# Optimization experiments

Hardware: AMD Instinct MI355X
Metric: run time of the kernel (lower is better)

The kernel has to match this reference:

```python
import jax, jax.numpy as jnp
import numpy as np

# Model/config constants
N = 2048          # total nodes in batch
G = 32            # number of graphs
NPG = 64          # nodes per graph (N = G * NPG)
E = 16384         # total edges (E//G per graph, unique within graph)
HIDDEN = 256
N_HEADS = 8
HEAD_DIM = HIDDEN // N_HEADS
EDGE_FEAT = 16
SCALE = HEAD_DIM ** -0.5


def setup_inputs() -> dict:
    key = jax.random.key(0)
    ks = jax.random.split(key, 16)
    nodes = jax.random.normal(ks[0], (N, HIDDEN), dtype=jnp.float32)
    edges = jax.random.normal(ks[1], (E, EDGE_FEAT), dtype=jnp.float32)
    n_node = jnp.full((G,), NPG, dtype=jnp.int32)
    # Unique (sender, receiver) pairs within each graph block
    epg = E // G
    gkeys = jax.random.split(ks[2], G)
    perm = jax.vmap(lambda k: jax.random.permutation(k, NPG * NPG)[:epg])(gkeys)  # [G, epg]
    so = perm // NPG
    ro = perm % NPG
    base = (jnp.arange(G, dtype=jnp.int32) * NPG)[:, None]
    senders = (base + so).reshape(-1).astype(jnp.int32)
    receivers = (base + ro).reshape(-1).astype(jnp.int32)
    init = 0.02
    Wq = jax.random.normal(ks[3], (HIDDEN, HIDDEN), jnp.float32) * init
    Wk = jax.random.normal(ks[4], (HIDDEN, HIDDEN), jnp.float32) * init
    Wv = jax.random.normal(ks[5], (HIDDEN, HIDDEN), jnp.float32) * init
    Wo = jax.random.normal(ks[6], (HIDDEN, HIDDEN), jnp.float32) * init
    We = jax.random.normal(ks[7], (EDGE_FEAT, N_HEADS), jnp.float32) * init
    bq = jnp.zeros((HIDDEN,), jnp.float32)
    bk = jnp.zeros((HIDDEN,), jnp.float32)
    bv = jnp.zeros((HIDDEN,), jnp.float32)
    bo = jnp.zeros((HIDDEN,), jnp.float32)
    be = jnp.zeros((N_HEADS,), jnp.float32)
    return {"nodes": nodes, "edges": edges, "n_node": n_node,
            "senders": senders, "receivers": receivers,
            "Wq": Wq, "bq": bq, "Wk": Wk, "bk": bk, "Wv": Wv, "bv": bv,
            "Wo": Wo, "bo": bo, "We": We, "be": be}


def reference(nodes, edges, n_node, senders, receivers,
              Wq, bq, Wk, bk, Wv, bv, Wo, bo, We, be):
    n_nodes = nodes.shape[0]
    n_graphs = n_node.shape[0]
    q = (nodes @ Wq + bq).reshape(n_nodes, N_HEADS, HEAD_DIM)
    k = (nodes @ Wk + bk).reshape(n_nodes, N_HEADS, HEAD_DIM)
    v = (nodes @ Wv + bv).reshape(n_nodes, N_HEADS, HEAD_DIM)
    scores = jnp.einsum('ihd,jhd->ijh', q, k) * SCALE  # [N, N, H]
    graph_idx = jnp.repeat(jnp.arange(n_graphs), n_node, total_repeat_length=n_nodes)
    same_graph = graph_idx[:, None] == graph_idx[None, :]
    scores = scores + jnp.where(same_graph[:, :, None], 0.0, -1e9)
    # Edge bias scattered into [N, N, H] at (receiver, sender)
    edge_bias = edges @ We + be  # [E, H]
    edge_bias_matrix = jnp.zeros((n_nodes, n_nodes, N_HEADS), dtype=scores.dtype)
    edge_bias_matrix = edge_bias_matrix.at[receivers, senders].set(edge_bias)
    scores = scores + edge_bias_matrix
    attn = jax.nn.softmax(scores, axis=1)  # softmax over key axis j
    out = jnp.einsum('ijh,jhd->ihd', attn, v).reshape(n_nodes, HIDDEN)
    return out @ Wo + bo
```

## Files before the change

### kernel.cpp

```cpp
#include <hip/hip_runtime.h>

#define N_NODES 2048
#define N_GRAPHS 32
#define NPG 64
#define N_EDGES 16384
#define EPG 512
#define HIDDEN 256
#define NHEADS 8
#define HEADDIM 32
#define EDGEFEAT 16
#define ATT_SCALE 0.17677669529663687f

typedef unsigned short u16;
typedef __attribute__((ext_vector_type(8))) short bf16x8;
typedef __attribute__((ext_vector_type(4))) float f32x4;

__device__ __forceinline__ u16 f2b(float f) {
    unsigned x = __float_as_uint(f);
    return (u16)((x + 0x7fffu + ((x >> 16) & 1u)) >> 16);
}
__device__ __forceinline__ float b2f(u16 u) {
    return __uint_as_float(((unsigned)u) << 16);
}
__device__ __forceinline__ unsigned pack2(float a, float b) {
    return (unsigned)f2b(a) | ((unsigned)f2b(b) << 16);
}

__global__ __launch_bounds__(256)
void qkv_attn_fused(const float* __restrict__ nodes,
                    const float* __restrict__ Wq, const float* __restrict__ Wk,
                    const float* __restrict__ Wv,
                    const float* __restrict__ bq, const float* __restrict__ bk,
                    const float* __restrict__ bv,
                    const float* __restrict__ edges, const float* __restrict__ We,
                    const float* __restrict__ be,
                    const int* __restrict__ senders, const int* __restrict__ receivers,
                    u16* __restrict__ attnb)
{
    const int g = blockIdx.x, h = blockIdx.y;
    const int tid = threadIdx.x;
    const int lane = tid & 63, wv = tid >> 6;
    const int l16 = lane & 15, quad = lane >> 4;

    __shared__ __align__(16) unsigned char smem[84480];
    short* An = (short*)smem;
    short* Wt = (short*)smem + 64 * 264;
    short* qhi = (short*)smem;
    short* qlo = qhi + 64 * 40;
    short* khi = qlo + 64 * 40;
    short* klo = khi + 64 * 40;
    short* vsT = klo + 64 * 40;
    float* sc  = (float*)(smem + 25088);
    float* red = sc + 64 * 65;
    __shared__ float we_h[EDGEFEAT];
    __shared__ float sbe;

    if (tid < EDGEFEAT) we_h[tid] = We[tid * NHEADS + h];
    if (tid == 0) sbe = be[h];

    #pragma unroll
    for (int rep = 0; rep < 16; ++rep) {
        const int q = rep * 256 + tid;
        const int row = q >> 6, f4 = q & 63;
        float4 x = *(const float4*)(nodes + (size_t)(g * NPG + row) * HIDDEN + f4 * 4);
        *(uint2*)&An[row * 264 + f4 * 4] = make_uint2(pack2(x.x, x.y), pack2(x.z, x.w));
    }
    #pragma unroll
    for (int rep = 0; rep < 24; ++rep) {
        const int q = rep * 256 + tid;
        const float* Wp = (rep < 8) ? Wq : (rep < 16) ? Wk : Wv;
        const int r = q & 2047;
        const int krow = r >> 3, f4 = r & 7;
        float4 x = *(const float4*)(Wp + (size_t)krow * HIDDEN + h * HEADDIM + f4 * 4);
        const int nb = (rep >> 3) * 32 + f4 * 4;
        Wt[(nb + 0) * 264 + krow] = (short)f2b(x.x);
        Wt[(nb + 1) * 264 + krow] = (short)f2b(x.y);
        Wt[(nb + 2) * 264 + krow] = (short)f2b(x.z);
        Wt[(nb + 3) * 264 + krow] = (short)f2b(x.w);
    }
    __syncthreads();

    f32x4 acc[6];
    #pragma unroll
    for (int nt = 0; nt < 6; ++nt) acc[nt] = (f32x4){0.f, 0.f, 0.f, 0.f};
    const int arow = (wv * 16 + l16) * 264 + quad * 8;
    #pragma unroll
    for (int k0 = 0; k0 < HIDDEN; k0 += 32) {
        bf16x8 af = *(const bf16x8*)&An[arow + k0];
        #pragma unroll
        for (int nt = 0; nt < 6; ++nt) {
            bf16x8 bf = *(const bf16x8*)&Wt[(nt * 16 + l16) * 264 + k0 + quad * 8];
            acc[nt] = __builtin_amdgcn_mfma_f32_16x16x32_bf16(af, bf, acc[nt], 0, 0, 0);
        }
    }
    __syncthreads();

    #pragma unroll
    for (int nt = 0; nt < 6; ++nt) {
        const int tns = nt >> 1;
        const int col = (nt & 1) * 16 + l16;
        const float* bp = (tns == 0) ? bq : (tns == 1) ? bk : bv;
        const float bias = bp[h * HEADDIM + col];
        #pragma unroll
        for (int r = 0; r < 4; ++r) {
            const int row = wv * 16 + quad * 4 + r;
            const float val = acc[nt][r] + bias;
            if (tns == 2) {
                vsT[col * 72 + row] = (short)f2b(val);
            } else {
                const u16 hi = f2b(val);
                const u16 lo = f2b(val - b2f(hi));
                if (tns == 0) { qhi[row * 40 + col] = (short)hi; qlo[row * 40 + col] = (short)lo; }
                else          { khi[row * 40 + col] = (short)hi; klo[row * 40 + col] = (short)lo; }
            }
        }
    }
    __syncthreads();

    {
        bf16x8 qh = *(const bf16x8*)&qhi[(wv * 16 + l16) * 40 + quad * 8];
        bf16x8 ql = *(const bf16x8*)&qlo[(wv * 16 + l16) * 40 + quad * 8];
        #pragma unroll
        for (int nt = 0; nt < 4; ++nt) {
            bf16x8 kh = *(const bf16x8*)&khi[(nt * 16 + l16) * 40 + quad * 8];
            bf16x8 kl = *(const bf16x8*)&klo[(nt * 16 + l16) * 40 + quad * 8];
            f32x4 s = (f32x4){0.f, 0.f, 0.f, 0.f};
            s = __builtin_amdgcn_mfma_f32_16x16x32_bf16(qh, kh, s, 0, 0, 0);
            s = __builtin_amdgcn_mfma_f32_16x16x32_bf16(qh, kl, s, 0, 0, 0);
            s = __builtin_amdgcn_mfma_f32_16x16x32_bf16(ql, kh, s, 0, 0, 0);
            #pragma unroll
            for (int r = 0; r < 4; ++r)
                sc[(wv * 16 + quad * 4 + r) * 65 + nt * 16 + l16] = s[r] * ATT_SCALE;
        }
    }
    __syncthreads();

    #pragma unroll
    for (int rep = 0; rep < 2; ++rep) {
        const int e = g * EPG + rep * 256 + tid;
        const float* ef = edges + (size_t)e * EDGEFEAT;
        float4 f0 = *(const float4*)(ef + 0);
        float4 f1 = *(const float4*)(ef + 4);
        float4 f2 = *(const float4*)(ef + 8);
        float4 f3 = *(const float4*)(ef + 12);
        float b = sbe
            + f0.x * we_h[0]  + f0.y * we_h[1]  + f0.z * we_h[2]  + f0.w * we_h[3]
            + f1.x * we_h[4]  + f1.y * we_h[5]  + f1.z * we_h[6]  + f1.w * we_h[7]
            + f2.x * we_h[8]  + f2.y * we_h[9]  + f2.z * we_h[10] + f2.w * we_h[11]
            + f3.x * we_h[12] + f3.y * we_h[13] + f3.z * we_h[14] + f3.w * we_h[15];
        const int s_l = senders[e] & (NPG - 1);
        const int r_l = receivers[e] & (NPG - 1);
        sc[r_l * 65 + s_l] += b;
    }
    __syncthreads();

    {
        const int i  = tid & 63;
        const int cg = tid >> 6;
        float* red_m = red;
        float* red_s = red + 4 * 64;
        float m = -1e30f;
        #pragma unroll
        for (int jj = 0; jj < 16; ++jj) m = fmaxf(m, sc[i * 65 + cg * 16 + jj]);
        red_m[cg * 64 + i] = m;
        __syncthreads();
        m = fmaxf(fmaxf(red_m[0 * 64 + i], red_m[1 * 64 + i]),
                  fmaxf(red_m[2 * 64 + i], red_m[3 * 64 + i]));
        float s = 0.f;
        #pragma unroll
        for (int jj = 0; jj < 16; ++jj) {
            const int j = cg * 16 + jj;
            float e = __expf(sc[i * 65 + j] - m);
            sc[i * 65 + j] = e;
            s += e;
        }
        red_s[cg * 64 + i] = s;
        __syncthreads();
        const float inv = 1.f / (red_s[0 * 64 + i] + red_s[1 * 64 + i] +
                                 red_s[2 * 64 + i] + red_s[3 * 64 + i]);
        #pragma unroll
        for (int jj = 0; jj < 16; ++jj) sc[i * 65 + cg * 16 + jj] *= inv;
    }
    __syncthreads();

    {
        f32x4 oacc[2];
        oacc[0] = (f32x4){0.f, 0.f, 0.f, 0.f};
        oacc[1] = (f32x4){0.f, 0.f, 0.f, 0.f};
        #pragma unroll
        for (int k0 = 0; k0 < NPG; k0 += 32) {
            float p[8];
            #pragma unroll
            for (int jj = 0; jj < 8; ++jj)
                p[jj] = sc[(wv * 16 + l16) * 65 + k0 + quad * 8 + jj];
            uint4 uh, ul;
            u16 h0 = f2b(p[0]), h1 = f2b(p[1]), h2 = f2b(p[2]), h3 = f2b(p[3]);
            u16 h4 = f2b(p[4]), h5 = f2b(p[5]), h6 = f2b(p[6]), h7 = f2b(p[7]);
            uh.x = (unsigned)h0 | ((unsigned)h1 << 16);
            uh.y = (unsigned)h2 | ((unsigned)h3 << 16);
            uh.z = (unsigned)h4 | ((unsigned)h5 << 16);
            uh.w = (unsigned)h6 | ((unsigned)h7 << 16);
            ul.x = pack2(p[0] - b2f(h0), p[1] - b2f(h1));
            ul.y = pack2(p[2] - b2f(h2), p[3] - b2f(h3));
            ul.z = pack2(p[4] - b2f(h4), p[5] - b2f(h5));
            ul.w = pack2(p[6] - b2f(h6), p[7] - b2f(h7));
            bf16x8 ph = *(bf16x8*)&uh;
            bf16x8 pl = *(bf16x8*)&ul;
            #pragma unroll
            for (int nt = 0; nt < 2; ++nt) {
                bf16x8 vf = *(const bf16x8*)&vsT[(nt * 16 + l16) * 72 + k0 + quad * 8];
                oacc[nt] = __builtin_amdgcn_mfma_f32_16x16x32_bf16(ph, vf, oacc[nt], 0, 0, 0);
                oacc[nt] = __builtin_amdgcn_mfma_f32_16x16x32_bf16(pl, vf, oacc[nt], 0, 0, 0);
            }
        }
        #pragma unroll
        for (int nt = 0; nt < 2; ++nt) {
            const int d = nt * 16 + l16;
            #pragma unroll
            for (int r = 0; r < 4; ++r) {
                const int row = wv * 16 + quad * 4 + r;
                attnb[(size_t)(g * NPG + row) * HIDDEN + h * HEADDIM + d] =
                    f2b(oacc[nt][r]);
            }
        }
    }
}

__global__ __launch_bounds__(256)
void outproj_fused(const u16* __restrict__ A,
                   const float* __restrict__ Wo,
                   const float* __restrict__ bo,
                   float* __restrict__ C)
{
    const int n0 = blockIdx.x * 64, m0 = blockIdx.y * 64;
    const int tid = threadIdx.x;
    const int lane = tid & 63, wv = tid >> 6;
    const int l16 = lane & 15, quad = lane >> 4;

    __shared__ __align__(16) short Ab[64 * 264];
    __shared__ __align__(16) short Bb[64 * 264];

    #pragma unroll
    for (int rep = 0; rep < 8; ++rep) {
        const int q = rep * 256 + tid;
        const int row = q >> 5, u = q & 31;
        *(uint4*)&Ab[row * 264 + u * 8] =
            *(const uint4*)(A + (size_t)(m0 + row) * HIDDEN + u * 8);
    }
    #pragma unroll
    for (int rep = 0; rep < 16; ++rep) {
        const int q = rep * 256 + tid;
        const int f4 = q & 7;
        const int krow = (q >> 3) & 255;
        const int half = q >> 11;
        float4 x = *(const float4*)(Wo + (size_t)krow * HIDDEN + n0 + half * 32 + f4 * 4);
        const int nb = half * 32 + f4 * 4;
        Bb[(nb + 0) * 264 + krow] = (short)f2b(x.x);
        Bb[(nb + 1) * 264 + krow] = (short)f2b(x.y);
        Bb[(nb + 2) * 264 + krow] = (short)f2b(x.z);
        Bb[(nb + 3) * 264 + krow] = (short)f2b(x.w);
    }
    __syncthreads();

    f32x4 acc[4];
    #pragma unroll
    for (int nt = 0; nt < 4; ++nt) acc[nt] = (f32x4){0.f, 0.f, 0.f, 0.f};
    const int arow = (wv * 16 + l16) * 264 + quad * 8;
    #pragma unroll
    for (int k0 = 0; k0 < HIDDEN; k0 += 32) {
        bf16x8 af = *(const bf16x8*)&Ab[arow + k0];
        #pragma unroll
        for (int nt = 0; nt < 4; ++nt) {
            bf16x8 bf = *(const bf16x8*)&Bb[(nt * 16 + l16) * 264 + k0 + quad * 8];
            acc[nt] = __builtin_amdgcn_mfma_f32_16x16x32_bf16(af, bf, acc[nt], 0, 0, 0);
        }
    }

    #pragma unroll
    for (int nt = 0; nt < 4; ++nt) {
        const int col = n0 + nt * 16 + l16;
        const float bias = bo[col];
        #pragma unroll
        for (int r = 0; r < 4; ++r)
            C[(size_t)(m0 + wv * 16 + quad * 4 + r) * HIDDEN + col] = acc[nt][r] + bias;
    }
}

extern "C" void kernel_launch(void* const* d_in, const int* in_sizes, int n_in,
                              void* d_out, int out_size, void* d_ws, size_t ws_size,
                              hipStream_t stream)
{
    const float* nodes     = (const float*)d_in[0];
    const float* edges     = (const float*)d_in[1];
    const int*   senders   = (const int*)d_in[3];
    const int*   receivers = (const int*)d_in[4];
    const float* Wq = (const float*)d_in[5];
    const float* bq = (const float*)d_in[6];
    const float* Wk = (const float*)d_in[7];
    const float* bk = (const float*)d_in[8];
    const float* Wv = (const float*)d_in[9];
    const float* bv = (const float*)d_in[10];
    const float* Wo = (const float*)d_in[11];
    const float* bo = (const float*)d_in[12];
    const float* We = (const float*)d_in[13];
    const float* be = (const float*)d_in[14];
    float* out = (float*)d_out;

    u16* attnb = (u16*)d_ws;

    qkv_attn_fused<<<dim3(N_GRAPHS, NHEADS), dim3(256), 0, stream>>>(
        nodes, Wq, Wk, Wv, bq, bk, bv, edges, We, be, senders, receivers, attnb);
    outproj_fused<<<dim3(HIDDEN / 64, N_NODES / 64), dim3(256), 0, stream>>>(
        attnb, Wo, bo, out);
}
```

Baseline: 93.70 us.

## Fuse attention and output projection into one cooperative kernel with grid sync

Merges the per-graph/head attention kernel and the output projection GEMM into a single cooperative launch of 256 blocks, separated by a grid-wide barrier. The second phase re-tiles the out-projection to 64x32 tiles so it uses the same 256 blocks. This removes one kernel launch and the inter-kernel gap, at the cost of a grid sync and smaller GEMM tiles that reload the A tile more often.

```diff
diff --git a/kernel.cpp b/kernel.cpp
--- a/kernel.cpp
+++ b/kernel.cpp
@@ -1,4 +1,7 @@
 #include <hip/hip_runtime.h>
+#include <hip/hip_cooperative_groups.h>
+
+namespace cg = cooperative_groups;
 
 #define N_NODES 2048
 #define N_GRAPHS 32
@@ -27,262 +30,263 @@
 }
 
 __global__ __launch_bounds__(256)
-void qkv_attn_fused(const float* __restrict__ nodes,
-                    const float* __restrict__ Wq, const float* __restrict__ Wk,
-                    const float* __restrict__ Wv,
-                    const float* __restrict__ bq, const float* __restrict__ bk,
-                    const float* __restrict__ bv,
-                    const float* __restrict__ edges, const float* __restrict__ We,
-                    const float* __restrict__ be,
-                    const int* __restrict__ senders, const int* __restrict__ receivers,
-                    u16* __restrict__ attnb)
+void fused_all(const float* __restrict__ nodes,
+               const float* __restrict__ Wq, const float* __restrict__ Wk,
+               const float* __restrict__ Wv,
+               const float* __restrict__ bq, const float* __restrict__ bk,
+               const float* __restrict__ bv,
+               const float* __restrict__ edges, const float* __restrict__ We,
+               const float* __restrict__ be,
+               const int* __restrict__ senders, const int* __restrict__ receivers,
+               const float* __restrict__ Wo, const float* __restrict__ bo,
+               u16* __restrict__ attnb,
+               float* __restrict__ out)
 {
-    const int g = blockIdx.x, h = blockIdx.y;
+    const int bid = blockIdx.x;
     const int tid = threadIdx.x;
     const int lane = tid & 63, wv = tid >> 6;
     const int l16 = lane & 15, quad = lane >> 4;
 
     __shared__ __align__(16) unsigned char smem[84480];
-    short* An = (short*)smem;
-    short* Wt = (short*)smem + 64 * 264;
-    short* qhi = (short*)smem;
-    short* qlo = qhi + 64 * 40;
-    short* khi = qlo + 64 * 40;
-    short* klo = khi + 64 * 40;
-    short* vsT = klo + 64 * 40;
-    float* sc  = (float*)(smem + 25088);
-    float* red = sc + 64 * 65;
     __shared__ float we_h[EDGEFEAT];
     __shared__ float sbe;
 
-    if (tid < EDGEFEAT) we_h[tid] = We[tid * NHEADS + h];
-    if (tid == 0) sbe = be[h];
-
-    #pragma unroll
-    for (int rep = 0; rep < 16; ++rep) {
-        const int q = rep * 256 + tid;
-        const int row = q >> 6, f4 = q & 63;
-        float4 x = *(const float4*)(nodes + (size_t)(g * NPG + row) * HIDDEN + f4 * 4);
-        *(uint2*)&An[row * 264 + f4 * 4] = make_uint2(pack2(x.x, x.y), pack2(x.z, x.w));
-    }
-    #pragma unroll
-    for (int rep = 0; rep < 24; ++rep) {
-        const int q = rep * 256 + tid;
-        const float* Wp = (rep < 8) ? Wq : (rep < 16) ? Wk : Wv;
-        const int r = q & 2047;
-        const int krow = r >> 3, f4 = r & 7;
-        float4 x = *(const float4*)(Wp + (size_t)krow * HIDDEN + h * HEADDIM + f4 * 4);
-        const int nb = (rep >> 3) * 32 + f4 * 4;
-        Wt[(nb + 0) * 264 + krow] = (short)f2b(x.x);
-        Wt[(nb + 1) * 264 + krow] = (short)f2b(x.y);
-        Wt[(nb + 2) * 264 + krow] = (short)f2b(x.z);
-        Wt[(nb + 3) * 264 + krow] = (short)f2b(x.w);
-    }
-    __syncthreads();
-
-    f32x4 acc[6];
-    #pragma unroll
-    for (int nt = 0; nt < 6; ++nt) acc[nt] = (f32x4){0.f, 0.f, 0.f, 0.f};
-    const int arow = (wv * 16 + l16) * 264 + quad * 8;
-    #pragma unroll
-    for (int k0 = 0; k0 < HIDDEN; k0 += 32) {
-        bf16x8 af = *(const bf16x8*)&An[arow + k0];
+    {
+        const int g = bid & 31, h = bid >> 5;
+
+        short* An = (short*)smem;
+        short* Wt = (short*)smem + 64 * 264;
+        short* qhi = (short*)smem;
+        short* qlo = qhi + 64 * 40;
+        short* khi = qlo + 64 * 40;
+        short* klo = khi + 64 * 40;
+        short* vsT = klo + 64 * 40;
+        float* sc  = (float*)(smem + 25088);
+        float* red = sc + 64 * 65;
+
+        if (tid < EDGEFEAT) we_h[tid] = We[tid * NHEADS + h];
+        if (tid == 0) sbe = be[h];
+
+        #pragma unroll
+        for (int rep = 0; rep < 16; ++rep) {
+            const int q = rep * 256 + tid;
+            const int row = q >> 6, f4 = q & 63;
+            float4 x = *(const float4*)(nodes + (size_t)(g * NPG + row) * HIDDEN + f4 * 4);
+            *(uint2*)&An[row * 264 + f4 * 4] = make_uint2(pack2(x.x, x.y), pack2(x.z, x.w));
+        }
+        #pragma unroll
+        for (int rep = 0; rep < 24; ++rep) {
+            const int q = rep * 256 + tid;
+            const float* Wp = (rep < 8) ? Wq : (rep < 16) ? Wk : Wv;
+            const int r = q & 2047;
+            const int krow = r >> 3, f4 = r & 7;
+            float4 x = *(const float4*)(Wp + (size_t)krow * HIDDEN + h * HEADDIM + f4 * 4);
+            const int nb = (rep >> 3) * 32 + f4 * 4;
+            Wt[(nb + 0) * 264 + krow] = (short)f2b(x.x);
+            Wt[(nb + 1) * 264 + krow] = (short)f2b(x.y);
+            Wt[(nb + 2) * 264 + krow] = (short)f2b(x.z);
+            Wt[(nb + 3) * 264 + krow] = (short)f2b(x.w);
+        }
+        __syncthreads();
+
+        f32x4 acc[6];
+        #pragma unroll
+        for (int nt = 0; nt < 6; ++nt) acc[nt] = (f32x4){0.f, 0.f, 0.f, 0.f};
+        const int arow = (wv * 16 + l16) * 264 + quad * 8;
+        #pragma unroll
+        for (int k0 = 0; k0 < HIDDEN; k0 += 32) {
+            bf16x8 af = *(const bf16x8*)&An[arow + k0];
+            #pragma unroll
+            for (int nt = 0; nt < 6; ++nt) {
+                bf16x8 bf = *(const bf16x8*)&Wt[(nt * 16 + l16) * 264 + k0 + quad * 8];
+                acc[nt] = __builtin_amdgcn_mfma_f32_16x16x32_bf16(af, bf, acc[nt], 0, 0, 0);
+            }
+        }
+        __syncthreads();
+
         #pragma unroll
         for (int nt = 0; nt < 6; ++nt) {
-            bf16x8 bf = *(const bf16x8*)&Wt[(nt * 16 + l16) * 264 + k0 + quad * 8];
-            acc[nt] = __builtin_amdgcn_mfma_f32_16x16x32_bf16(af, bf, acc[nt], 0, 0, 0);
-        }
-    }
-    __syncthreads();
-
-    #pragma unroll
-    for (int nt = 0; nt < 6; ++nt) {
-        const int tns = nt >> 1;
-        const int col = (nt & 1) * 16 + l16;
-        const float* bp = (tns == 0) ? bq : (tns == 1) ? bk : bv;
-        const float bias = bp[h * HEADDIM + col];
-        #pragma unroll
-        for (int r = 0; r < 4; ++r) {
-            const int row = wv * 16 + quad * 4 + r;
-            const float val = acc[nt][r] + bias;
-            if (tns == 2) {
-                vsT[col * 72 + row] = (short)f2b(val);
-            } else {
-                const u16 hi = f2b(val);
-                const u16 lo = f2b(val - b2f(hi));
-                if (tns == 0) { qhi[row * 40 + col] = (short)hi; qlo[row * 40 + col] = (short)lo; }
-                else          { khi[row * 40 + col] = (short)hi; klo[row * 40 + col] = (short)lo; }
-            }
-        }
-    }
-    __syncthreads();
-
-    {
-        bf16x8 qh = *(const bf16x8*)&qhi[(wv * 16 + l16) * 40 + quad * 8];
-        bf16x8 ql = *(const bf16x8*)&qlo[(wv * 16 + l16) * 40 + quad * 8];
-        #pragma unroll
-        for (int nt = 0; nt < 4; ++nt) {
-            bf16x8 kh = *(const bf16x8*)&khi[(nt * 16 + l16) * 40 + quad * 8];
-            bf16x8 kl = *(const bf16x8*)&klo[(nt * 16 + l16) * 40 + quad * 8];
-            f32x4 s = (f32x4){0.f, 0.f, 0.f, 0.f};
-            s = __builtin_amdgcn_mfma_f32_16x16x32_bf16(qh, kh, s, 0, 0, 0);
-            s = __builtin_amdgcn_mfma_f32_16x16x32_bf16(qh, kl, s, 0, 0, 0);
-            s = __builtin_amdgcn_mfma_f32_16x16x32_bf16(ql, kh, s, 0, 0, 0);
-            #pragma unroll
-            for (int r = 0; r < 4; ++r)
-                sc[(wv * 16 + quad * 4 + r) * 65 + nt * 16 + l16] = s[r] * ATT_SCALE;
-        }
-    }
-    __syncthreads();
-
-    #pragma unroll
-    for (int rep = 0; rep < 2; ++rep) {
-        const int e = g * EPG + rep * 256 + tid;
-        const float* ef = edges + (size_t)e * EDGEFEAT;
-        float4 f0 = *(const float4*)(ef + 0);
-        float4 f1 = *(const float4*)(ef + 4);
-        float4 f2 = *(const float4*)(ef + 8);
-        float4 f3 = *(const float4*)(ef + 12);
-        float b = sbe
-            + f0.x * we_h[0]  + f0.y * we_h[1]  + f0.z * we_h[2]  + f0.w * we_h[3]
-            + f1.x * we_h[4]  + f1.y * we_h[5]  + f1.z * we_h[6]  + f1.w * we_h[7]
-            + f2.x * we_h[8]  + f2.y * we_h[9]  + f2.z * we_h[10] + f2.w * we_h[11]
-            + f3.x * we_h[12] + f3.y * we_h[13] + f3.z * we_h[14] + f3.w * we_h[15];
-        const int s_l = senders[e] & (NPG - 1);
-        const int r_l = receivers[e] & (NPG - 1);
-        sc[r_l * 65 + s_l] += b;
-    }
-    __syncthreads();
-
-    {
-        const int i  = tid & 63;
-        const int cg = tid >> 6;
-        float* red_m = red;
-        float* red_s = red + 4 * 64;
-        float m = -1e30f;
-        #pragma unroll
-        for (int jj = 0; jj < 16; ++jj) m = fmaxf(m, sc[i * 65 + cg * 16 + jj]);
-        red_m[cg * 64 + i] = m;
-        __syncthreads();
-        m = fmaxf(fmaxf(red_m[0 * 64 + i], red_m[1 * 64 + i]),
-                  fmaxf(red_m[2 * 64 + i], red_m[3 * 64 + i]));
-        float s = 0.f;
-        #pragma unroll
-        for (int jj = 0; jj < 16; ++jj) {
-            const int j = cg * 16 + jj;
-            float e = __expf(sc[i * 65 + j] - m);
-            sc[i * 65 + j] = e;
-            s += e;
-        }
-        red_s[cg * 64 + i] = s;
-        __syncthreads();
-        const float inv = 1.f / (red_s[0 * 64 + i] + red_s[1 * 64 + i] +
-                                 red_s[2 * 64 + i] + red_s[3 * 64 + i]);
-        #pragma unroll
-        for (int jj = 0; jj < 16; ++jj) sc[i * 65 + cg * 16 + jj] *= inv;
-    }
-    __syncthreads();
-
-    {
-        f32x4 oacc[2];
-        oacc[0] = (f32x4){0.f, 0.f, 0.f, 0.f};
-        oacc[1] = (f32x4){0.f, 0.f, 0.f, 0.f};
-        #pragma unroll
-        for (int k0 = 0; k0 < NPG; k0 += 32) {
-            float p[8];
-            #pragma unroll
-            for (int jj = 0; jj < 8; ++jj)
-                p[jj] = sc[(wv * 16 + l16) * 65 + k0 + quad * 8 + jj];
-            uint4 uh, ul;
-            u16 h0 = f2b(p[0]), h1 = f2b(p[1]), h2 = f2b(p[2]), h3 = f2b(p[3]);
-            u16 h4 = f2b(p[4]), h5 = f2b(p[5]), h6 = f2b(p[6]), h7 = f2b(p[7]);
-            uh.x = (unsigned)h0 | ((unsigned)h1 << 16);
-            uh.y = (unsigned)h2 | ((unsigned)h3 << 16);
-            uh.z = (unsigned)h4 | ((unsigned)h5 << 16);
-            uh.w = (unsigned)h6 | ((unsigned)h7 << 16);
-            ul.x = pack2(p[0] - b2f(h0), p[1] - b2f(h1));
-            ul.y = pack2(p[2] - b2f(h2), p[3] - b2f(h3));
-            ul.z = pack2(p[4] - b2f(h4), p[5] - b2f(h5));
-            ul.w = pack2(p[6] - b2f(h6), p[7] - b2f(h7));
-            bf16x8 ph = *(bf16x8*)&uh;
-            bf16x8 pl = *(bf16x8*)&ul;
-            #pragma unroll
-            for (int nt = 0; nt < 2; ++nt) {
-                bf16x8 vf = *(const bf16x8*)&vsT[(nt * 16 + l16) * 72 + k0 + quad * 8];
-                oacc[nt] = __builtin_amdgcn_mfma_f32_16x16x32_bf16(ph, vf, oacc[nt], 0, 0, 0);
-                oacc[nt] = __builtin_amdgcn_mfma_f32_16x16x32_bf16(pl, vf, oacc[nt], 0, 0, 0);
-            }
-        }
-        #pragma unroll
-        for (int nt = 0; nt < 2; ++nt) {
-            const int d = nt * 16 + l16;
+            const int tns = nt >> 1;
+            const int col = (nt & 1) * 16 + l16;
+            const float* bp = (tns == 0) ? bq : (tns == 1) ? bk : bv;
+            const float bias = bp[h * HEADDIM + col];
             #pragma unroll
             for (int r = 0; r < 4; ++r) {
                 const int row = wv * 16 + quad * 4 + r;
-                attnb[(size_t)(g * NPG + row) * HIDDEN + h * HEADDIM + d] =
-                    f2b(oacc[nt][r]);
+                const float val = acc[nt][r] + bias;
+                if (tns == 2) {
+                    vsT[col * 72 + row] = (short)f2b(val);
+                } else {
+                    const u16 hi = f2b(val);
+                    const u16 lo = f2b(val - b2f(hi));
+                    if (tns == 0) { qhi[row * 40 + col] = (short)hi; qlo[row * 40 + col] = (short)lo; }
+                    else          { khi[row * 40 + col] = (short)hi; klo[row * 40 + col] = (short)lo; }
+                }
+            }
+        }
+        __syncthreads();
+
+        {
+            bf16x8 qh = *(const bf16x8*)&qhi[(wv * 16 + l16) * 40 + quad * 8];
+            bf16x8 ql = *(const bf16x8*)&qlo[(wv * 16 + l16) * 40 + quad * 8];
+            #pragma unroll
+            for (int nt = 0; nt < 4; ++nt) {
+                bf16x8 kh = *(const bf16x8*)&khi[(nt * 16 + l16) * 40 + quad * 8];
+                bf16x8 kl = *(const bf16x8*)&klo[(nt * 16 + l16) * 40 + quad * 8];
+                f32x4 s = (f32x4){0.f, 0.f, 0.f, 0.f};
+                s = __builtin_amdgcn_mfma_f32_16x16x32_bf16(qh, kh, s, 0, 0, 0);
+                s = __builtin_amdgcn_mfma_f32_16x16x32_bf16(qh, kl, s, 0, 0, 0);
+                s = __builtin_amdgcn_mfma_f32_16x16x32_bf16(ql, kh, s, 0, 0, 0);
+                #pragma unroll
+                for (int r = 0; r < 4; ++r)
+                    sc[(wv * 16 + quad * 4 + r) * 65 + nt * 16 + l16] = s[r] * ATT_SCALE;
+            }
+        }
+        __syncthreads();
+
+        #pragma unroll
+        for (int rep = 0; rep < 2; ++rep) {
+            const int e = g * EPG + rep * 256 + tid;
+            const float* ef = edges + (size_t)e * EDGEFEAT;
+            float4 f0 = *(const float4*)(ef + 0);
+            float4 f1 = *(const float4*)(ef + 4);
+            float4 f2 = *(const float4*)(ef + 8);
+            float4 f3 = *(const float4*)(ef + 12);
+            float b = sbe
+                + f0.x * we_h[0]  + f0.y * we_h[1]  + f0.z * we_h[2]  + f0.w * we_h[3]
+                + f1.x * we_h[4]  + f1.y * we_h[5]  + f1.z * we_h[6]  + f1.w * we_h[7]
+                + f2.x * we_h[8]  + f2.y * we_h[9]  + f2.z * we_h[10] + f2.w * we_h[11]
+                + f3.x * we_h[12] + f3.y * we_h[13] + f3.z * we_h[14] + f3.w * we_h[15];
+            const int s_l = senders[e] & (NPG - 1);
+            const int r_l = receivers[e] & (NPG - 1);
+            sc[r_l * 65 + s_l] += b;
+        }
+        __syncthreads();
+
+        {
+            const int i  = tid & 63;
+            const int cg_ = tid >> 6;
+            float* red_m = red;
+            float* red_s = red + 4 * 64;
+            float m = -1e30f;
+            #pragma unroll
+            for (int jj = 0; jj < 16; ++jj) m = fmaxf(m, sc[i * 65 + cg_ * 16 + jj]);
+            red_m[cg_ * 64 + i] = m;
+            __syncthreads();
+            m = fmaxf(fmaxf(red_m[0 * 64 + i], red_m[1 * 64 + i]),
+                      fmaxf(red_m[2 * 64 + i], red_m[3 * 64 + i]));
+            float s = 0.f;
+            #pragma unroll
+            for (int jj = 0; jj < 16; ++jj) {
+                const int j = cg_ * 16 + jj;
+                float e = __expf(sc[i * 65 + j] - m);
+                sc[i * 65 + j] = e;
+                s += e;
+            }
+            red_s[cg_ * 64 + i] = s;
+            __syncthreads();
+            const float inv = 1.f / (red_s[0 * 64 + i] + red_s[1 * 64 + i] +
+                                     red_s[2 * 64 + i] + red_s[3 * 64 + i]);
+            #pragma unroll
+            for (int jj = 0; jj < 16; ++jj) sc[i * 65 + cg_ * 16 + jj] *= inv;
+        }
+        __syncthreads();
+
+        {
+            f32x4 oacc[2];
+            oacc[0] = (f32x4){0.f, 0.f, 0.f, 0.f};
+            oacc[1] = (f32x4){0.f, 0.f, 0.f, 0.f};
+            #pragma unroll
+            for (int k0 = 0; k0 < NPG; k0 += 32) {
+                float p[8];
+                #pragma unroll
+                for (int jj = 0; jj < 8; ++jj)
+                    p[jj] = sc[(wv * 16 + l16) * 65 + k0 + quad * 8 + jj];
+                uint4 uh, ul;
+                u16 h0 = f2b(p[0]), h1 = f2b(p[1]), h2 = f2b(p[2]), h3 = f2b(p[3]);
+                u16 h4 = f2b(p[4]), h5 = f2b(p[5]), h6 = f2b(p[6]), h7 = f2b(p[7]);
+                uh.x = (unsigned)h0 | ((unsigned)h1 << 16);
+                uh.y = (unsigned)h2 | ((unsigned)h3 << 16);
+                uh.z = (unsigned)h4 | ((unsigned)h5 << 16);
+                uh.w = (unsigned)h6 | ((unsigned)h7 << 16);
+                ul.x = pack2(p[0] - b2f(h0), p[1] - b2f(h1));
+                ul.y = pack2(p[2] - b2f(h2), p[3] - b2f(h3));
+                ul.z = pack2(p[4] - b2f(h4), p[5] - b2f(h5));
+                ul.w = pack2(p[6] - b2f(h6), p[7] - b2f(h7));
+                bf16x8 ph = *(bf16x8*)&uh;
+                bf16x8 pl = *(bf16x8*)&ul;
+                #pragma unroll
+                for (int nt = 0; nt < 2; ++nt) {
+                    bf16x8 vf = *(const bf16x8*)&vsT[(nt * 16 + l16) * 72 + k0 + quad * 8];
+                    oacc[nt] = __builtin_amdgcn_mfma_f32_16x16x32_bf16(ph, vf, oacc[nt], 0, 0, 0);
+                    oacc[nt] = __builtin_amdgcn_mfma_f32_16x16x32_bf16(pl, vf, oacc[nt], 0, 0, 0);
+                }
+            }
+            #pragma unroll
+            for (int nt = 0; nt < 2; ++nt) {
+                const int d = nt * 16 + l16;
+                #pragma unroll
+                for (int r = 0; r < 4; ++r) {
+                    const int row = wv * 16 + quad * 4 + r;
+                    attnb[(size_t)(g * NPG + row) * HIDDEN + h * HEADDIM + d] =
+                        f2b(oacc[nt][r]);
+                }
             }
         }
     }
-}
-
-__global__ __launch_bounds__(256)
-void outproj_fused(const u16* __restrict__ A,
-                   const float* __restrict__ Wo,
-                   const float* __restrict__ bo,
-                   float* __restrict__ C)
-{
-    const int n0 = blockIdx.x * 64, m0 = blockIdx.y * 64;
-    const int tid = threadIdx.x;
-    const int lane = tid & 63, wv = tid >> 6;
-    const int l16 = lane & 15, quad = lane >> 4;
-
-    __shared__ __align__(16) short Ab[64 * 264];
-    __shared__ __align__(16) short Bb[64 * 264];
-
-    #pragma unroll
-    for (int rep = 0; rep < 8; ++rep) {
-        const int q = rep * 256 + tid;
-        const int row = q >> 5, u = q & 31;
-        *(uint4*)&Ab[row * 264 + u * 8] =
-            *(const uint4*)(A + (size_t)(m0 + row) * HIDDEN + u * 8);
-    }
-    #pragma unroll
-    for (int rep = 0; rep < 16; ++rep) {
-        const int q = rep * 256 + tid;
-        const int f4 = q & 7;
-        const int krow = (q >> 3) & 255;
-        const int half = q >> 11;
-        float4 x = *(const float4*)(Wo + (size_t)krow * HIDDEN + n0 + half * 32 + f4 * 4);
-        const int nb = half * 32 + f4 * 4;
-        Bb[(nb + 0) * 264 + krow] = (short)f2b(x.x);
-        Bb[(nb + 1) * 264 + krow] = (short)f2b(x.y);
-        Bb[(nb + 2) * 264 + krow] = (short)f2b(x.z);
-        Bb[(nb + 3) * 264 + krow] = (short)f2b(x.w);
-    }
-    __syncthreads();
-
-    f32x4 acc[4];
-    #pragma unroll
-    for (int nt = 0; nt < 4; ++nt) acc[nt] = (f32x4){0.f, 0.f, 0.f, 0.f};
-    const int arow = (wv * 16 + l16) * 264 + quad * 8;
-    #pragma unroll
-    for (int k0 = 0; k0 < HIDDEN; k0 += 32) {
-        bf16x8 af = *(const bf16x8*)&Ab[arow + k0];
-        #pragma unroll
-        for (int nt = 0; nt < 4; ++nt) {
-            bf16x8 bf = *(const bf16x8*)&Bb[(nt * 16 + l16) * 264 + k0 + quad * 8];
-            acc[nt] = __builtin_amdgcn_mfma_f32_16x16x32_bf16(af, bf, acc[nt], 0, 0, 0);
-        }
-    }
-
-    #pragma unroll
-    for (int nt = 0; nt < 4; ++nt) {
-        const int col = n0 + nt * 16 + l16;
-        const float bias = bo[col];
-        #pragma unroll
-        for (int r = 0; r < 4; ++r)
-            C[(size_t)(m0 + wv * 16 + quad * 4 + r) * HIDDEN + col] = acc[nt][r] + bias;
+
+    cg::this_grid().sync();
+
+    {
+        const int m0 = (bid & 31) * 64;
+        const int n0 = (bid >> 5) * 32;
+
+        short* Ab = (short*)smem;
+        short* Bb = (short*)smem + 64 * 264;
+
+        #pragma unroll
+        for (int rep = 0; rep < 8; ++rep) {
+            const int q = rep * 256 + tid;
+            const int row = q >> 5, u = q & 31;
+            *(uint4*)&Ab[row * 264 + u * 8] =
+                *(const uint4*)(attnb + (size_t)(m0 + row) * HIDDEN + u * 8);
+        }
+        #pragma unroll
+        for (int rep = 0; rep < 8; ++rep) {
+            const int q = rep * 256 + tid;
+            const int krow = q >> 3, f4 = q & 7;
+            float4 x = *(const float4*)(Wo + (size_t)krow * HIDDEN + n0 + f4 * 4);
+            const int nb = f4 * 4;
+            Bb[(nb + 0) * 264 + krow] = (short)f2b(x.x);
+            Bb[(nb + 1) * 264 + krow] = (short)f2b(x.y);
+            Bb[(nb + 2) * 264 + krow] = (short)f2b(x.z);
+            Bb[(nb + 3) * 264 + krow] = (short)f2b(x.w);
+        }
+        __syncthreads();
+
+        f32x4 acc[2];
+        acc[0] = (f32x4){0.f, 0.f, 0.f, 0.f};
+        acc[1] = (f32x4){0.f, 0.f, 0.f, 0.f};
+        const int arow = (wv * 16 + l16) * 264 + quad * 8;
+        #pragma unroll
+        for (int k0 = 0; k0 < HIDDEN; k0 += 32) {
+            bf16x8 af = *(const bf16x8*)&Ab[arow + k0];
+            #pragma unroll
+            for (int nt = 0; nt < 2; ++nt) {
+                bf16x8 bf = *(const bf16x8*)&Bb[(nt * 16 + l16) * 264 + k0 + quad * 8];
+                acc[nt] = __builtin_amdgcn_mfma_f32_16x16x32_bf16(af, bf, acc[nt], 0, 0, 0);
+            }
+        }
+
+        #pragma unroll
+        for (int nt = 0; nt < 2; ++nt) {
+            const int col = n0 + nt * 16 + l16;
+            const float bias = bo[col];
+            #pragma unroll
+            for (int r = 0; r < 4; ++r)
+                out[(size_t)(m0 + wv * 16 + quad * 4 + r) * HIDDEN + col] =
+                    acc[nt][r] + bias;
+        }
     }
 }
 
@@ -308,8 +312,13 @@
 
     u16* attnb = (u16*)d_ws;
 
-    qkv_attn_fused<<<dim3(N_GRAPHS, NHEADS), dim3(256), 0, stream>>>(
-        nodes, Wq, Wk, Wv, bq, bk, bv, edges, We, be, senders, receivers, attnb);
-    outproj_fused<<<dim3(HIDDEN / 64, N_NODES / 64), dim3(256), 0, stream>>>(
-        attnb, Wo, bo, out);
-}
+    void* args[] = {
+        (void*)&nodes, (void*)&Wq, (void*)&Wk, (void*)&Wv,
+        (void*)&bq, (void*)&bk, (void*)&bv,
+        (void*)&edges, (void*)&We, (void*)&be,
+        (void*)&senders, (void*)&receivers,
+        (void*)&Wo, (void*)&bo, (void*)&attnb, (void*)&out
+    };
+    hipLaunchCooperativeKernel((const void*)fused_all, dim3(256), dim3(256),
+                               args, 0, stream);
+}
```

After: 151.2 us. +61.3%, slower.

## Load node fragments directly into registers and prefetch edge data early

Applied to the files above, without the earlier changes.

The QKV projection now builds the bf16 A fragments straight from global memory into registers, so the node tile is no longer staged through shared memory. That staging cut lets the LDS allocation shrink. Edge features and sender/receiver indices are loaded at kernel start so their latency overlaps the weight staging and the matmuls. Shared-memory strides for the transposed weight and V tiles change to odd-word padding (266/74) to reduce bank conflicts on the transposed stores. The risk is that 16-byte vector LDS reads at those strides are no longer 16-byte aligned, and more registers stay live.

```diff
diff --git a/kernel.cpp b/kernel.cpp
--- a/kernel.cpp
+++ b/kernel.cpp
@@ -10,6 +10,10 @@
 #define HEADDIM 32
 #define EDGEFEAT 16
 #define ATT_SCALE 0.17677669529663687f
+
+#define WT_S 266
+#define VS_S 74
+#define QK_S 40
 
 typedef unsigned short u16;
 typedef __attribute__((ext_vector_type(8))) short bf16x8;
@@ -42,15 +46,14 @@
     const int lane = tid & 63, wv = tid >> 6;
     const int l16 = lane & 15, quad = lane >> 4;
 
-    __shared__ __align__(16) unsigned char smem[84480];
-    short* An = (short*)smem;
-    short* Wt = (short*)smem + 64 * 264;
+    __shared__ __align__(16) unsigned char smem[51072 + 128];
+    short* Wt  = (short*)smem;
     short* qhi = (short*)smem;
-    short* qlo = qhi + 64 * 40;
-    short* khi = qlo + 64 * 40;
-    short* klo = khi + 64 * 40;
-    short* vsT = klo + 64 * 40;
-    float* sc  = (float*)(smem + 25088);
+    short* qlo = qhi + 64 * QK_S;
+    short* khi = qlo + 64 * QK_S;
+    short* klo = khi + 64 * QK_S;
+    short* vsT = klo + 64 * QK_S;
+    float* sc  = (float*)(smem + 25600);
     float* red = sc + 64 * 65;
     __shared__ float we_h[EDGEFEAT];
     __shared__ float sbe;
@@ -58,13 +61,33 @@
     if (tid < EDGEFEAT) we_h[tid] = We[tid * NHEADS + h];
     if (tid == 0) sbe = be[h];
 
-    #pragma unroll
-    for (int rep = 0; rep < 16; ++rep) {
-        const int q = rep * 256 + tid;
-        const int row = q >> 6, f4 = q & 63;
-        float4 x = *(const float4*)(nodes + (size_t)(g * NPG + row) * HIDDEN + f4 * 4);
-        *(uint2*)&An[row * 264 + f4 * 4] = make_uint2(pack2(x.x, x.y), pack2(x.z, x.w));
-    }
+    bf16x8 aF[8];
+    {
+        const float* ag = nodes + (size_t)(g * NPG + wv * 16 + l16) * HIDDEN + quad * 8;
+        #pragma unroll
+        for (int t = 0; t < 8; ++t) {
+            float4 x0 = *(const float4*)(ag + t * 32);
+            float4 x1 = *(const float4*)(ag + t * 32 + 4);
+            uint4 u;
+            u.x = pack2(x0.x, x0.y); u.y = pack2(x0.z, x0.w);
+            u.z = pack2(x1.x, x1.y); u.w = pack2(x1.z, x1.w);
+            aF[t] = *(bf16x8*)&u;
+        }
+    }
+    float4 ef[2][4];
+    int es[2], er[2];
+    #pragma unroll
+    for (int rep = 0; rep < 2; ++rep) {
+        const int e = g * EPG + rep * 256 + tid;
+        const float* ep = edges + (size_t)e * EDGEFEAT;
+        ef[rep][0] = *(const float4*)(ep + 0);
+        ef[rep][1] = *(const float4*)(ep + 4);
+        ef[rep][2] = *(const float4*)(ep + 8);
+        ef[rep][3] = *(const float4*)(ep + 12);
+        es[rep] = senders[e] & (NPG - 1);
+        er[rep] = receivers[e] & (NPG - 1);
+    }
+
     #pragma unroll
     for (int rep = 0; rep < 24; ++rep) {
         const int q = rep * 256 + tid;
@@ -73,24 +96,23 @@
         const int krow = r >> 3, f4 = r & 7;
         float4 x = *(const float4*)(Wp + (size_t)krow * HIDDEN + h * HEADDIM + f4 * 4);
         const int nb = (rep >> 3) * 32 + f4 * 4;
-        Wt[(nb + 0) * 264 + krow] = (short)f2b(x.x);
-        Wt[(nb + 1) * 264 + krow] = (short)f2b(x.y);
-        Wt[(nb + 2) * 264 + krow] = (short)f2b(x.z);
-        Wt[(nb + 3) * 264 + krow] = (short)f2b(x.w);
+        Wt[(nb + 0) * WT_S + krow] = (short)f2b(x.x);
+        Wt[(nb + 1) * WT_S + krow] = (short)f2b(x.y);
+        Wt[(nb + 2) * WT_S + krow] = (short)f2b(x.z);
+        Wt[(nb + 3) * WT_S + krow] = (short)f2b(x.w);
     }
     __syncthreads();
 
     f32x4 acc[6];
     #pragma unroll
     for (int nt = 0; nt < 6; ++nt) acc[nt] = (f32x4){0.f, 0.f, 0.f, 0.f};
-    const int arow = (wv * 16 + l16) * 264 + quad * 8;
-    #pragma unroll
-    for (int k0 = 0; k0 < HIDDEN; k0 += 32) {
-        bf16x8 af = *(const bf16x8*)&An[arow + k0];
+    #pragma unroll
+    for (int t = 0; t < 8; ++t) {
+        const int k0 = t * 32;
         #pragma unroll
         for (int nt = 0; nt < 6; ++nt) {
-            bf16x8 bf = *(const bf16x8*)&Wt[(nt * 16 + l16) * 264 + k0 + quad * 8];
-            acc[nt] = __builtin_amdgcn_mfma_f32_16x16x32_bf16(af, bf, acc[nt], 0, 0, 0);
+            bf16x8 bf = *(const bf16x8*)&Wt[(nt * 16 + l16) * WT_S + k0 + quad * 8];
+            acc[nt] = __builtin_amdgcn_mfma_f32_16x16x32_bf16(aF[t], bf, acc[nt], 0, 0, 0);
         }
     }
     __syncthreads();
@@ -106,24 +128,24 @@
             const int row = wv * 16 + quad * 4 + r;
             const float val = acc[nt][r] + bias;
             if (tns == 2) {
-                vsT[col * 72 + row] = (short)f2b(val);
+                vsT[col * VS_S + row] = (short)f2b(val);
             } else {
                 const u16 hi = f2b(val);
                 const u16 lo = f2b(val - b2f(hi));
-                if (tns == 0) { qhi[row * 40 + col] = (short)hi; qlo[row * 40 + col] = (short)lo; }
-                else          { khi[row * 40 + col] = (short)hi; klo[row * 40 + col] = (short)lo; }
+                if (tns == 0) { qhi[row * QK_S + col] = (short)hi; qlo[row * QK_S + col] = (short)lo; }
+                else          { khi[row * QK_S + col] = (short)hi; klo[row * QK_S + col] = (short)lo; }
             }
         }
     }
     __syncthreads();
 
     {
-        bf16x8 qh = *(const bf16x8*)&qhi[(wv * 16 + l16) * 40 + quad * 8];
-        bf16x8 ql = *(const bf16x8*)&qlo[(wv * 16 + l16) * 40 + quad * 8];
+        bf16x8 qh = *(const bf16x8*)&qhi[(wv * 16 + l16) * QK_S + quad * 8];
+        bf16x8 ql = *(const bf16x8*)&qlo[(wv * 16 + l16) * QK_S + quad * 8];
         #pragma unroll
         for (int nt = 0; nt < 4; ++nt) {
-            bf16x8 kh = *(const bf16x8*)&khi[(nt * 16 + l16) * 40 + quad * 8];
-            bf16x8 kl = *(const bf16x8*)&klo[(nt * 16 + l16) * 40 + quad * 8];
+            bf16x8 kh = *(const bf16x8*)&khi[(nt * 16 + l16) * QK_S + quad * 8];
+            bf16x8 kl = *(const bf16x8*)&klo[(nt * 16 + l16) * QK_S + quad * 8];
             f32x4 s = (f32x4){0.f, 0.f, 0.f, 0.f};
             s = __builtin_amdgcn_mfma_f32_16x16x32_bf16(qh, kh, s, 0, 0, 0);
             s = __builtin_amdgcn_mfma_f32_16x16x32_bf16(qh, kl, s, 0, 0, 0);
@@ -137,49 +159,45 @@
 
     #pragma unroll
     for (int rep = 0; rep < 2; ++rep) {
-        const int e = g * EPG + rep * 256 + tid;
-        const float* ef = edges + (size_t)e * EDGEFEAT;
-        float4 f0 = *(const float4*)(ef + 0);
-        float4 f1 = *(const float4*)(ef + 4);
-        float4 f2 = *(const float4*)(ef + 8);
-        float4 f3 = *(const float4*)(ef + 12);
         float b = sbe
-            + f0.x * we_h[0]  + f0.y * we_h[1]  + f0.z * we_h[2]  + f0.w * we_h[3]
-            + f1.x * we_h[4]  + f1.y * we_h[5]  + f1.z * we_h[6]  + f1.w * we_h[7]
-            + f2.x * we_h[8]  + f2.y * we_h[9]  + f2.z * we_h[10] + f2.w * we_h[11]
-            + f3.x * we_h[12] + f3.y * we_h[13] + f3.z * we_h[14] + f3.w * we_h[15];
-        const int s_l = senders[e] & (NPG - 1);
-        const int r_l = receivers[e] & (NPG - 1);
-        sc[r_l * 65 + s_l] += b;
+            + ef[rep][0].x * we_h[0]  + ef[rep][0].y * we_h[1]
+            + ef[rep][0].z * we_h[2]  + ef[rep][0].w * we_h[3]
+            + ef[rep][1].x * we_h[4]  + ef[rep][1].y * we_h[5]
+            + ef[rep][1].z * we_h[6]  + ef[rep][1].w * we_h[7]
+            + ef[rep][2].x * we_h[8]  + ef[rep][2].y * we_h[9]
+            + ef[rep][2].z * we_h[10] + ef[rep][2].w * we_h[11]
+            + ef[rep][3].x * we_h[12] + ef[rep][3].y * we_h[13]
+            + ef[rep][3].z * we_h[14] + ef[rep][3].w * we_h[15];
+        sc[er[rep] * 65 + es[rep]] += b;
     }
     __syncthreads();
 
     {
         const int i  = tid & 63;
-        const int cg = tid >> 6;
+        const int cg_ = tid >> 6;
         float* red_m = red;
         float* red_s = red + 4 * 64;
         float m = -1e30f;
         #pragma unroll
-        for (int jj = 0; jj < 16; ++jj) m = fmaxf(m, sc[i * 65 + cg * 16 + jj]);
-        red_m[cg * 64 + i] = m;
+        for (int jj = 0; jj < 16; ++jj) m = fmaxf(m, sc[i * 65 + cg_ * 16 + jj]);
+        red_m[cg_ * 64 + i] = m;
         __syncthreads();
         m = fmaxf(fmaxf(red_m[0 * 64 + i], red_m[1 * 64 + i]),
                   fmaxf(red_m[2 * 64 + i], red_m[3 * 64 + i]));
         float s = 0.f;
         #pragma unroll
         for (int jj = 0; jj < 16; ++jj) {
-            const int j = cg * 16 + jj;
+            const int j = cg_ * 16 + jj;
             float e = __expf(sc[i * 65 + j] - m);
             sc[i * 65 + j] = e;
             s += e;
         }
-        red_s[cg * 64 + i] = s;
+        red_s[cg_ * 64 + i] = s;
         __syncthreads();
         const float inv = 1.f / (red_s[0 * 64 + i] + red_s[1 * 64 + i] +
                                  red_s[2 * 64 + i] + red_s[3 * 64 + i]);
         #pragma unroll
-        for (int jj = 0; jj < 16; ++jj) sc[i * 65 + cg * 16 + jj] *= inv;
+        for (int jj = 0; jj < 16; ++jj) sc[i * 65 + cg_ * 16 + jj] *= inv;
     }
     __syncthreads();
 
@@ -208,7 +226,7 @@
             bf16x8 pl = *(bf16x8*)&ul;
             #pragma unroll
             for (int nt = 0; nt < 2; ++nt) {
-                bf16x8 vf = *(const bf16x8*)&vsT[(nt * 16 + l16) * 72 + k0 + quad * 8];
+                bf16x8 vf = *(const bf16x8*)&vsT[(nt * 16 + l16) * VS_S + k0 + quad * 8];
                 oacc[nt] = __builtin_amdgcn_mfma_f32_16x16x32_bf16(ph, vf, oacc[nt], 0, 0, 0);
                 oacc[nt] = __builtin_amdgcn_mfma_f32_16x16x32_bf16(pl, vf, oacc[nt], 0, 0, 0);
             }
@@ -238,7 +256,7 @@
     const int l16 = lane & 15, quad = lane >> 4;
 
     __shared__ __align__(16) short Ab[64 * 264];
-    __shared__ __align__(16) short Bb[64 * 264];
+    __shared__ __align__(16) short Bb[64 * WT_S];
 
     #pragma unroll
     for (int rep = 0; rep < 8; ++rep) {
@@ -255,10 +273,10 @@
         const int half = q >> 11;
         float4 x = *(const float4*)(Wo + (size_t)krow * HIDDEN + n0 + half * 32 + f4 * 4);
         const int nb = half * 32 + f4 * 4;
-        Bb[(nb + 0) * 264 + krow] = (short)f2b(x.x);
-        Bb[(nb + 1) * 264 + krow] = (short)f2b(x.y);
-        Bb[(nb + 2) * 264 + krow] = (short)f2b(x.z);
-        Bb[(nb + 3) * 264 + krow] = (short)f2b(x.w);
+        Bb[(nb + 0) * WT_S + krow] = (short)f2b(x.x);
+        Bb[(nb + 1) * WT_S + krow] = (short)f2b(x.y);
+        Bb[(nb + 2) * WT_S + krow] = (short)f2b(x.z);
+        Bb[(nb + 3) * WT_S + krow] = (short)f2b(x.w);
     }
     __syncthreads();
 
@@ -271,7 +289,7 @@
         bf16x8 af = *(const bf16x8*)&Ab[arow + k0];
         #pragma unroll
         for (int nt = 0; nt < 4; ++nt) {
-            bf16x8 bf = *(const bf16x8*)&Bb[(nt * 16 + l16) * 264 + k0 + quad * 8];
+            bf16x8 bf = *(const bf16x8*)&Bb[(nt * 16 + l16) * WT_S + k0 + quad * 8];
             acc[nt] = __builtin_amdgcn_mfma_f32_16x16x32_bf16(af, bf, acc[nt], 0, 0, 0);
         }
     }
```

Result: slower. 107.6 us (+14.9%).

## Pack weight transposes into 32-bit LDS stores and halve out-proj tile width

Applied to the files above, without the earlier changes.

The weight staging loops in both kernels now load two consecutive k-rows at once and write packed bf16 pairs with 32-bit LDS stores, where before they issued four scattered 16-bit stores per element group. The aim is to cut LDS store instruction count and bank conflicts in the transpose. The output projection also switches from 64-wide to 32-wide column tiles, which doubles its grid from 128 to 256 blocks to fill more CUs. The cost is that each A tile is loaded twice as often.

```diff
diff --git a/kernel.cpp b/kernel.cpp
--- a/kernel.cpp
+++ b/kernel.cpp
@@ -66,17 +66,21 @@
         *(uint2*)&An[row * 264 + f4 * 4] = make_uint2(pack2(x.x, x.y), pack2(x.z, x.w));
     }
     #pragma unroll
-    for (int rep = 0; rep < 24; ++rep) {
+    for (int rep = 0; rep < 12; ++rep) {
         const int q = rep * 256 + tid;
-        const float* Wp = (rep < 8) ? Wq : (rep < 16) ? Wk : Wv;
-        const int r = q & 2047;
-        const int krow = r >> 3, f4 = r & 7;
-        float4 x = *(const float4*)(Wp + (size_t)krow * HIDDEN + h * HEADDIM + f4 * 4);
-        const int nb = (rep >> 3) * 32 + f4 * 4;
-        Wt[(nb + 0) * 264 + krow] = (short)f2b(x.x);
-        Wt[(nb + 1) * 264 + krow] = (short)f2b(x.y);
-        Wt[(nb + 2) * 264 + krow] = (short)f2b(x.z);
-        Wt[(nb + 3) * 264 + krow] = (short)f2b(x.w);
+        const float* Wp = (rep < 4) ? Wq : (rep < 8) ? Wk : Wv;
+        const int tns = (rep < 4) ? 0 : (rep < 8) ? 1 : 2;
+        const int r = q & 1023;
+        const int kpair = r >> 3, f4 = r & 7;
+        const int krow = kpair * 2;
+        const float* src = Wp + (size_t)krow * HIDDEN + h * HEADDIM + f4 * 4;
+        float4 x0 = *(const float4*)(src);
+        float4 x1 = *(const float4*)(src + HIDDEN);
+        const int nb = tns * 32 + f4 * 4;
+        *(unsigned*)&Wt[(nb + 0) * 264 + krow] = pack2(x0.x, x1.x);
+        *(unsigned*)&Wt[(nb + 1) * 264 + krow] = pack2(x0.y, x1.y);
+        *(unsigned*)&Wt[(nb + 2) * 264 + krow] = pack2(x0.z, x1.z);
+        *(unsigned*)&Wt[(nb + 3) * 264 + krow] = pack2(x0.w, x1.w);
     }
     __syncthreads();
 
@@ -232,13 +236,13 @@
                    const float* __restrict__ bo,
                    float* __restrict__ C)
 {
-    const int n0 = blockIdx.x * 64, m0 = blockIdx.y * 64;
+    const int n0 = blockIdx.x * 32, m0 = blockIdx.y * 64;
     const int tid = threadIdx.x;
     const int lane = tid & 63, wv = tid >> 6;
     const int l16 = lane & 15, quad = lane >> 4;
 
     __shared__ __align__(16) short Ab[64 * 264];
-    __shared__ __align__(16) short Bb[64 * 264];
+    __shared__ __align__(16) short Bb[32 * 264];
 
     #pragma unroll
     for (int rep = 0; rep < 8; ++rep) {
@@ -248,36 +252,37 @@
             *(const uint4*)(A + (size_t)(m0 + row) * HIDDEN + u * 8);
     }
     #pragma unroll
-    for (int rep = 0; rep < 16; ++rep) {
+    for (int rep = 0; rep < 4; ++rep) {
         const int q = rep * 256 + tid;
-        const int f4 = q & 7;
-        const int krow = (q >> 3) & 255;
-        const int half = q >> 11;
-        float4 x = *(const float4*)(Wo + (size_t)krow * HIDDEN + n0 + half * 32 + f4 * 4);
-        const int nb = half * 32 + f4 * 4;
-        Bb[(nb + 0) * 264 + krow] = (short)f2b(x.x);
-        Bb[(nb + 1) * 264 + krow] = (short)f2b(x.y);
-        Bb[(nb + 2) * 264 + krow] = (short)f2b(x.z);
-        Bb[(nb + 3) * 264 + krow] = (short)f2b(x.w);
-    }
-    __syncthreads();
-
-    f32x4 acc[4];
-    #pragma unroll
-    for (int nt = 0; nt < 4; ++nt) acc[nt] = (f32x4){0.f, 0.f, 0.f, 0.f};
+        const int kpair = q >> 3, f4 = q & 7;
+        const int krow = kpair * 2;
+        const float* src = Wo + (size_t)krow * HIDDEN + n0 + f4 * 4;
+        float4 x0 = *(const float4*)(src);
+        float4 x1 = *(const float4*)(src + HIDDEN);
+        const int nb = f4 * 4;
+        *(unsigned*)&Bb[(nb + 0) * 264 + krow] = pack2(x0.x, x1.x);
+        *(unsigned*)&Bb[(nb + 1) * 264 + krow] = pack2(x0.y, x1.y);
+        *(unsigned*)&Bb[(nb + 2) * 264 + krow] = pack2(x0.z, x1.z);
+        *(unsigned*)&Bb[(nb + 3) * 264 + krow] = pack2(x0.w, x1.w);
+    }
+    __syncthreads();
+
+    f32x4 acc[2];
+    acc[0] = (f32x4){0.f, 0.f, 0.f, 0.f};
+    acc[1] = (f32x4){0.f, 0.f, 0.f, 0.f};
     const int arow = (wv * 16 + l16) * 264 + quad * 8;
     #pragma unroll
     for (int k0 = 0; k0 < HIDDEN; k0 += 32) {
         bf16x8 af = *(const bf16x8*)&Ab[arow + k0];
         #pragma unroll
-        for (int nt = 0; nt < 4; ++nt) {
+        for (int nt = 0; nt < 2; ++nt) {
             bf16x8 bf = *(const bf16x8*)&Bb[(nt * 16 + l16) * 264 + k0 + quad * 8];
             acc[nt] = __builtin_amdgcn_mfma_f32_16x16x32_bf16(af, bf, acc[nt], 0, 0, 0);
         }
     }
 
     #pragma unroll
-    for (int nt = 0; nt < 4; ++nt) {
+    for (int nt = 0; nt < 2; ++nt) {
         const int col = n0 + nt * 16 + l16;
         const float bias = bo[col];
         #pragma unroll
@@ -310,6 +315,6 @@
 
     qkv_attn_fused<<<dim3(N_GRAPHS, NHEADS), dim3(256), 0, stream>>>(
         nodes, Wq, Wk, Wv, bq, bk, bv, edges, We, be, senders, receivers, attnb);
-    outproj_fused<<<dim3(HIDDEN / 64, N_NODES / 64), dim3(256), 0, stream>>>(
+    outproj_fused<<<dim3(HIDDEN / 32, N_NODES / 64), dim3(256), 0, stream>>>(
         attnb, Wo, bo, out);
 }
```

After: 95.38 us. No clear change (+1.8%).
